# Optimization experiments

Measured on AMD Instinct MI355X. Metric: run time of the kernel, lower is better.

Reference implementation:

```python
import jax, jax.numpy as jnp
import numpy as np

D_MODEL = 2048
N_HEADS = 16
D_HEAD = D_MODEL // N_HEADS
B, S = 4, 2048


def setup_inputs() -> dict:
    key = jax.random.key(0)
    ks = jax.random.split(key, 5)
    scale = 1.0 / np.sqrt(D_MODEL)
    return {
        "x": jax.random.normal(ks[0], (B, S, D_MODEL), dtype=jnp.float32),
        "w_qkv": jax.random.normal(ks[1], (D_MODEL, 3 * D_MODEL), dtype=jnp.float32) * scale,
        "b_qkv": jax.random.normal(ks[2], (3 * D_MODEL,), dtype=jnp.float32) * 0.01,
        "w_out": jax.random.normal(ks[3], (D_MODEL, D_MODEL), dtype=jnp.float32) * scale,
        "b_out": jax.random.normal(ks[4], (D_MODEL,), dtype=jnp.float32) * 0.01,
    }


def reference(x, w_qkv, b_qkv, w_out, b_out):
    b, s, d = x.shape
    qkv = x @ w_qkv + b_qkv                      # [b, s, 3d]
    q, k, v = jnp.split(qkv, 3, axis=-1)
    # [b, h, s, dh]
    q = q.reshape(b, s, N_HEADS, D_HEAD).transpose(0, 2, 1, 3)
    k = k.reshape(b, s, N_HEADS, D_HEAD).transpose(0, 2, 1, 3)
    v = v.reshape(b, s, N_HEADS, D_HEAD).transpose(0, 2, 1, 3)
    # past_kv is None -> s_past == s
    scale = 1.0 / np.sqrt(D_HEAD).astype(np.float32)
    scores = jnp.einsum("bhqd,bhkd->bhqk", q, k) * scale  # [b, h, s, s]
    # causal mask: disallow j > i (diagonal = 1 + s_past - s = 1)
    causal = jnp.tril(jnp.ones((s, s), dtype=bool))
    scores = jnp.where(causal, scores, jnp.float32(-jnp.inf))
    attn = jax.nn.softmax(scores, axis=-1)
    out = jnp.einsum("bhqk,bhkd->bhqd", attn, v)          # [b, h, s, dh]
    out = out.transpose(0, 2, 1, 3).reshape(b, s, d)
    out = out @ w_out + b_out
    return out, k, v
```

## Files before the change

kernel.cpp:

```cpp
#include <hip/hip_runtime.h>
#include <hip/hip_bf16.h>
#include <cstdint>

typedef unsigned short u16;
typedef unsigned int u32;
typedef __attribute__((ext_vector_type(4))) float f32x4;
typedef __attribute__((ext_vector_type(8))) __bf16 bf16x8;

#define DEVFN static __device__ __forceinline__

constexpr int Bb = 4, S = 2048, Dm = 2048, H = 16, DH = 128;
constexpr int M  = Bb * S;
constexpr int N3 = 3 * Dm;
constexpr int KK = 2048;
constexpr float ATTN_SCALE = 0.088388347648318447f;
constexpr float LOG2E = 1.4426950408889634f;

DEVFN u16 f2bf(float f) {
  union { float f; u32 u; } v; v.f = f;
  u32 u = v.u;
  return (u16)((u + 0x7fffu + ((u >> 16) & 1u)) >> 16);
}

DEVFN void async16(const void* g, void* l) {
  __builtin_amdgcn_global_load_lds(
      (__attribute__((address_space(1))) unsigned int*)(g),
      (__attribute__((address_space(3))) unsigned int*)(l), 16, 0, 0);
}


__global__ __launch_bounds__(256) void k_cvt_bf16(const float* __restrict__ in,
                                                  u16* __restrict__ out, int n) {
  int i = (blockIdx.x * 256 + threadIdx.x) * 4;
  if (i < n) {
    float4 f = *(const float4*)(in + i);
    ushort4 o;
    o.x = f2bf(f.x); o.y = f2bf(f.y); o.z = f2bf(f.z); o.w = f2bf(f.w);
    *(ushort4*)(out + i) = o;
  }
}

__global__ __launch_bounds__(256) void k_transpose_bf16(const float* __restrict__ in,
                                                        u16* __restrict__ out,
                                                        int R, int C) {
  __shared__ float tile[32][33];
  int c0 = blockIdx.x * 32, r0 = blockIdx.y * 32;
  int tx = threadIdx.x & 31, ty = threadIdx.x >> 5;
#pragma unroll
  for (int i = 0; i < 4; i++)
    tile[ty + 8 * i][tx] = in[(size_t)(r0 + ty + 8 * i) * C + c0 + tx];
  __syncthreads();
#pragma unroll
  for (int i = 0; i < 4; i++)
    out[(size_t)(c0 + ty + 8 * i) * R + r0 + tx] = f2bf(tile[tx][ty + 8 * i]);
}


#define RA(buf, half) ((buf) * 65536 + (half) * 16384)
#define RB(buf, half) ((buf) * 65536 + 32768 + (half) * 16384)

#define BARRIER() __builtin_amdgcn_s_barrier()
#define LGK0() asm volatile("s_waitcnt lgkmcnt(0)" ::: "memory")
#define VM6() asm volatile("s_waitcnt vmcnt(6)" ::: "memory")
#define VM0() asm volatile("s_waitcnt vmcnt(0)" ::: "memory")

template <int BUF>
DEVFN void ldAall(const char* lds, int wm, int lrow, int lkg, bf16x8 af[2][4][2]) {
  const char* base = lds + RA(BUF, 0) + wm * 16384;
  const int sw = (lrow & 7) << 4;
#pragma unroll
  for (int ms = 0; ms < 2; ms++)
#pragma unroll
    for (int mi = 0; mi < 4; mi++) {
      int row = ms * 64 + mi * 16 + lrow;
#pragma unroll
      for (int kk = 0; kk < 2; kk++)
        af[ms][mi][kk] = *(const bf16x8*)(base + row * 128 +
                                          ((kk * 64 + lkg * 16) ^ sw));
    }
}

template <int BUF, int NS>
DEVFN void ldB(const char* lds, int wn, int lrow, int lkg, bf16x8 b[2][2]) {
  const char* base = lds + RB(BUF, 0) + (wn >> 1) * 16384;
  const int sw = (lrow & 7) << 4;
#pragma unroll
  for (int ni = 0; ni < 2; ni++) {
    int row = (wn & 1) * 64 + NS * 32 + ni * 16 + lrow;
#pragma unroll
    for (int kk = 0; kk < 2; kk++)
      b[ni][kk] = *(const bf16x8*)(base + row * 128 +
                                   ((kk * 64 + lkg * 16) ^ sw));
  }
}

template <int MS, int NS>
DEVFN void mmq(f32x4 acc[8][4], bf16x8 af[4][2], bf16x8 b[2][2]) {
  __builtin_amdgcn_s_setprio(1);
#pragma unroll
  for (int kk = 0; kk < 2; kk++)
#pragma unroll
    for (int mi = 0; mi < 4; mi++)
#pragma unroll
      for (int ni = 0; ni < 2; ni++)
        acc[MS * 4 + mi][NS * 2 + ni] = __builtin_amdgcn_mfma_f32_16x16x32_bf16(
            af[mi][kk], b[ni][kk], acc[MS * 4 + mi][NS * 2 + ni], 0, 0, 0);
  __builtin_amdgcn_s_setprio(0);
}

#define STAGE0(ptr, region)                                             \
  {                                                                     \
    const u16* _q = (ptr);                                              \
    async16(_q, ldsc + (region) + dstoff);                              \
    async16(_q + (size_t)64 * KK, ldsc + (region) + 8192 + dstoff);     \
  }
#define STAGE(p, region) { STAGE0(p, region); p += 64; }

template <int MODE>
__global__ __launch_bounds__(512, 2) void k_gemm(
    const u16* __restrict__ A, const u16* __restrict__ BT,
    const float* __restrict__ bias, float* __restrict__ Cf,
    u16* __restrict__ q_bf, u16* __restrict__ k_bf, u16* __restrict__ v_bfT,
    int N) {
  __shared__ __align__(16) char lds[131072];
  char* ldsc = lds;
  const int tid = threadIdx.x;
  const int wid = tid >> 6, lane = tid & 63;
  const int wm = wid >> 2, wn = wid & 3;
  const int lrow = lane & 15, lkg = lane >> 4;

  const int bid = blockIdx.x;
  const int xcd = bid & 7;
  const int i = bid >> 3;
  const int r = i & 15;
  const int j = i >> 4;
  const int tm0 = (xcd * 4 + (r >> 2)) << 8;
  const int tn0 = (j * 4 + (r & 3)) << 8;

  const int NT = KK >> 6;

  const int srow = tid >> 3;
  const int scol = (((tid & 7) * 16) ^ ((srow & 7) << 4)) >> 1;
  const int dstoff = (tid & ~63) * 16;
  const u16* bA0 = A + (size_t)(tm0 + srow) * KK + scol;
  const u16* bA1 = A + (size_t)(tm0 + 128 + srow) * KK + scol;
  const u16* bB0 = BT + (size_t)(tn0 + srow) * KK + scol;
  const u16* bB1 = BT + (size_t)(tn0 + 128 + srow) * KK + scol;

  f32x4 acc[8][4] = {};

  STAGE0(bA0, RA(0, 0));
  STAGE0(bA1, RA(0, 1));
  STAGE0(bB0, RB(0, 0));
  STAGE0(bB1, RB(0, 1));
  STAGE0(bA0 + 64, RA(1, 0));
  STAGE0(bA1 + 64, RA(1, 1));
  STAGE0(bB0 + 64, RB(1, 0));
  VM6();
  BARRIER();

  const u16* pB1 = bB1 + 64;
  const u16* pA0 = bA0 + 128;
  const u16* pA1 = bA1 + 128;
  const u16* pB0 = bB0 + 128;

  for (int it = 0; it < NT / 2; it++) {
    bf16x8 af[2][4][2], b0[2][2], b1[2][2];

    ldAall<0>(ldsc, wm, lrow, lkg, af);
    ldB<0, 0>(ldsc, wn, lrow, lkg, b0);
    STAGE(pB1, RB(1, 1));
    BARRIER(); LGK0();
    mmq<0, 0>(acc, af[0], b0);
    BARRIER();

    ldB<0, 1>(ldsc, wn, lrow, lkg, b1);
    STAGE(pA0, RA(0, 0));
    BARRIER(); LGK0();
    mmq<0, 1>(acc, af[0], b1);
    BARRIER();

    STAGE(pA1, RA(0, 1));
    BARRIER();
    mmq<1, 0>(acc, af[1], b0);
    BARRIER();

    STAGE(pB0, RB(0, 0));
    VM6();
    BARRIER();
    mmq<1, 1>(acc, af[1], b1);
    BARRIER();

    ldAall<1>(ldsc, wm, lrow, lkg, af);
    ldB<1, 0>(ldsc, wn, lrow, lkg, b0);
    STAGE(pB1, RB(0, 1));
    BARRIER(); LGK0();
    mmq<0, 0>(acc, af[0], b0);
    BARRIER();

    ldB<1, 1>(ldsc, wn, lrow, lkg, b1);
    STAGE(pA0, RA(1, 0));
    BARRIER(); LGK0();
    mmq<0, 1>(acc, af[0], b1);
    BARRIER();

    STAGE(pA1, RA(1, 1));
    BARRIER();
    mmq<1, 0>(acc, af[1], b0);
    BARRIER();

    STAGE(pB0, RB(1, 0));
    VM6();
    BARRIER();
    mmq<1, 1>(acc, af[1], b1);
    BARRIER();
  }
  VM0();

  if (MODE == 0) {
#pragma unroll
    for (int mig = 0; mig < 8; mig++) {
      int row = tm0 + wm * 128 + (mig >> 2) * 64 + (mig & 3) * 16 + lkg * 4;
#pragma unroll
      for (int nig = 0; nig < 4; nig++) {
        int col = tn0 + wn * 64 + (nig >> 1) * 32 + (nig & 1) * 16 + lrow;
        float bv = bias[col];
#pragma unroll
        for (int r2 = 0; r2 < 4; r2++)
          Cf[(size_t)(row + r2) * N + col] = acc[mig][nig][r2] + bv;
      }
    }
  } else {
#pragma unroll
    for (int mig = 0; mig < 8; mig++) {
      int row = tm0 + wm * 128 + (mig >> 2) * 64 + (mig & 3) * 16 + lkg * 4;
#pragma unroll
      for (int nig = 0; nig < 4; nig++) {
        int n = tn0 + wn * 64 + (nig >> 1) * 32 + (nig & 1) * 16 + lrow;
        float bv = bias[n];
        int type = n >> 11;
        int d = n & 2047;
        int h = d >> 7, dh = d & 127;
#pragma unroll
        for (int r2 = 0; r2 < 4; r2++) {
          int rr = row + r2;
          int b = rr >> 11, s = rr & 2047;
          float val = acc[mig][nig][r2] + bv;
          size_t idx = ((size_t)(b * H + h) * S + s) * DH + dh;
          if (type == 0) {
            q_bf[idx] = f2bf(val * ATTN_SCALE);
          } else if (type == 1) {
            Cf[(size_t)M * Dm + idx] = val;
            k_bf[idx] = f2bf(val);
          } else {
            Cf[(size_t)2 * M * Dm + idx] = val;
            v_bfT[((size_t)(b * H + h) * DH + dh) * S + s] = f2bf(val);
          }
        }
      }
    }
  }
}

__global__ __launch_bounds__(256, 2) void k_attn(const u16* __restrict__ q_bf,
                                                 const u16* __restrict__ k_bf,
                                                 const u16* __restrict__ v_bfT,
                                                 u16* __restrict__ attn_bf) {
  __shared__ u16 ldsK[2][64 * 128];
  __shared__ u16 ldsV[2][128 * 64];
  __shared__ u16 ldsP[4][32 * 64];

  const int tid = threadIdx.x;
  const int wid = tid >> 6, lane = tid & 63;
  const int lrow = lane & 15, lkg = lane >> 4;

  const int bid = blockIdx.x;
  const int xcd = bid & 7;
  const int ii = bid >> 3;
  const int bh = xcd * 8 + (ii >> 4);
  const int qi = 15 - (ii & 15);
  const int b = bh >> 4, h = bh & 15;
  const int wq0 = qi * 128 + wid * 32;
  const int swz = (lrow & 7) << 4;

  const u16* qp = q_bf + (size_t)bh * S * DH;
  const u16* kp = k_bf + (size_t)bh * S * DH;
  const u16* vp = v_bfT + (size_t)bh * DH * S;

  bf16x8 qf[2][4];
#pragma unroll
  for (int qt = 0; qt < 2; qt++)
#pragma unroll
    for (int kk = 0; kk < 4; kk++)
      qf[qt][kk] = *(const bf16x8*)(qp + (size_t)(wq0 + qt * 16 + lrow) * DH +
                                    kk * 32 + lkg * 8);

  float mr[2][4], lr[2][4];
#pragma unroll
  for (int qt = 0; qt < 2; qt++)
#pragma unroll
    for (int r = 0; r < 4; r++) { mr[qt][r] = -1e30f; lr[qt][r] = 0.f; }
  f32x4 oacc[2][8] = {};

  const int nkb = qi * 2 + 2;

  auto stage = [&](int kb, int buf) {
#pragma unroll
    for (int i = 0; i < 4; i++) {
      int L = i * 4096 + wid * 1024 + lane * 16;
      int krow = L >> 8, kch = (L >> 4) & 15;
      async16(kp + (size_t)(kb * 64 + krow) * DH + ((kch ^ (krow & 7)) * 8),
              (char*)ldsK[buf] + L);
      int vd = L >> 7, vch = (L >> 4) & 7;
      async16(vp + (size_t)vd * S + kb * 64 + ((vch ^ (vd & 7)) * 8),
              (char*)ldsV[buf] + L);
    }
  };

  stage(0, 0);
  asm volatile("s_waitcnt vmcnt(0)" ::: "memory");
  __builtin_amdgcn_s_barrier();

  int cur = 0;
  for (int kb = 0; kb < nkb; kb++) {
    if (kb + 1 < nkb) stage(kb + 1, cur ^ 1);

    if (kb * 64 <= wq0 + 31) {
      const u16* Kc = ldsK[cur];
      const u16* Vc = ldsV[cur];
      f32x4 sacc[2][4] = {};
      __builtin_amdgcn_s_setprio(1);
#pragma unroll
      for (int kt = 0; kt < 4; kt++)
#pragma unroll
        for (int kk = 0; kk < 4; kk++) {
          bf16x8 kf = *(const bf16x8*)((const char*)Kc +
                        (kt * 16 + lrow) * 256 + ((kk * 64 + lkg * 16) ^ swz));
          sacc[0][kt] = __builtin_amdgcn_mfma_f32_16x16x32_bf16(qf[0][kk], kf,
                                                                sacc[0][kt], 0, 0, 0);
          sacc[1][kt] = __builtin_amdgcn_mfma_f32_16x16x32_bf16(qf[1][kk], kf,
                                                                sacc[1][kt], 0, 0, 0);
        }
      __builtin_amdgcn_s_setprio(0);

      if (kb * 64 + 63 > wq0) {
#pragma unroll
        for (int qt = 0; qt < 2; qt++)
#pragma unroll
          for (int kt = 0; kt < 4; kt++) {
            int k = kb * 64 + kt * 16 + lrow;
#pragma unroll
            for (int r = 0; r < 4; r++)
              if (k > wq0 + qt * 16 + lkg * 4 + r) sacc[qt][kt][r] = -1e30f;
          }
      }

      float pm[2][4];
#pragma unroll
      for (int qt = 0; qt < 2; qt++)
#pragma unroll
        for (int r = 0; r < 4; r++)
          pm[qt][r] = fmaxf(fmaxf(sacc[qt][0][r], sacc[qt][1][r]),
                            fmaxf(sacc[qt][2][r], sacc[qt][3][r]));
#pragma unroll
      for (int off = 1; off < 16; off <<= 1)
#pragma unroll
        for (int qt = 0; qt < 2; qt++)
#pragma unroll
          for (int r = 0; r < 4; r++)
            pm[qt][r] = fmaxf(pm[qt][r], __shfl_xor(pm[qt][r], off, 64));

      float dmax = pm[0][0] - mr[0][0];
#pragma unroll
      for (int qt = 0; qt < 2; qt++)
#pragma unroll
        for (int r = 0; r < 4; r++)
          dmax = fmaxf(dmax, pm[qt][r] - mr[qt][r]);
      if (!__all(dmax <= 8.0f)) {
        float sc[2][4];
#pragma unroll
        for (int qt = 0; qt < 2; qt++)
#pragma unroll
          for (int r = 0; r < 4; r++) {
            float mn = fmaxf(mr[qt][r], pm[qt][r]);
            sc[qt][r] = exp2f((mr[qt][r] - mn) * LOG2E);
            mr[qt][r] = mn;
            lr[qt][r] *= sc[qt][r];
          }
#pragma unroll
        for (int qt = 0; qt < 2; qt++)
#pragma unroll
          for (int nd = 0; nd < 8; nd++)
#pragma unroll
            for (int r = 0; r < 4; r++) oacc[qt][nd][r] *= sc[qt][r];
      }

      float rs[2][4] = {};
#pragma unroll
      for (int qt = 0; qt < 2; qt++)
#pragma unroll
        for (int kt = 0; kt < 4; kt++)
#pragma unroll
          for (int r = 0; r < 4; r++) {
            float p = exp2f((sacc[qt][kt][r] - mr[qt][r]) * LOG2E);
            rs[qt][r] += p;
            int prow = qt * 16 + lkg * 4 + r;
            *(u16*)((char*)ldsP[wid] + prow * 128 +
                    (((kt * 16 + lrow) * 2) ^ ((prow & 7) << 4))) = f2bf(p);
          }
#pragma unroll
      for (int off = 1; off < 16; off <<= 1)
#pragma unroll
        for (int qt = 0; qt < 2; qt++)
#pragma unroll
          for (int r = 0; r < 4; r++)
            rs[qt][r] += __shfl_xor(rs[qt][r], off, 64);
#pragma unroll
      for (int qt = 0; qt < 2; qt++)
#pragma unroll
        for (int r = 0; r < 4; r++)
          lr[qt][r] += rs[qt][r];

      asm volatile("s_waitcnt lgkmcnt(0)" ::: "memory");
      bf16x8 pf[2][2];
#pragma unroll
      for (int qt = 0; qt < 2; qt++)
#pragma unroll
        for (int kk = 0; kk < 2; kk++)
          pf[qt][kk] = *(const bf16x8*)((const char*)ldsP[wid] +
                         (qt * 16 + lrow) * 128 + ((kk * 64 + lkg * 16) ^ swz));
      __builtin_amdgcn_s_setprio(1);
#pragma unroll
      for (int nd = 0; nd < 8; nd++) {
        bf16x8 vf0 = *(const bf16x8*)((const char*)Vc +
                       (nd * 16 + lrow) * 128 + ((lkg * 16) ^ swz));
        bf16x8 vf1 = *(const bf16x8*)((const char*)Vc +
                       (nd * 16 + lrow) * 128 + ((64 + lkg * 16) ^ swz));
#pragma unroll
        for (int qt = 0; qt < 2; qt++) {
          oacc[qt][nd] = __builtin_amdgcn_mfma_f32_16x16x32_bf16(pf[qt][0], vf0,
                                                                 oacc[qt][nd], 0, 0, 0);
          oacc[qt][nd] = __builtin_amdgcn_mfma_f32_16x16x32_bf16(pf[qt][1], vf1,
                                                                 oacc[qt][nd], 0, 0, 0);
        }
      }
      __builtin_amdgcn_s_setprio(0);
    }

    asm volatile("s_waitcnt vmcnt(0)" ::: "memory");
    __builtin_amdgcn_s_barrier();
    cur ^= 1;
  }

#pragma unroll
  for (int qt = 0; qt < 2; qt++) {
    float inv[4];
#pragma unroll
    for (int r = 0; r < 4; r++) inv[r] = 1.0f / lr[qt][r];
#pragma unroll
    for (int nd = 0; nd < 8; nd++)
#pragma unroll
      for (int r = 0; r < 4; r++) {
        int q = wq0 + qt * 16 + lkg * 4 + r;
        size_t idx = ((size_t)(b * S + q) * H + h) * DH + nd * 16 + lrow;
        attn_bf[idx] = f2bf(oacc[qt][nd][r] * inv[r]);
      }
  }
}


extern "C" void kernel_launch(void* const* d_in, const int* in_sizes, int n_in,
                              void* d_out, int out_size, void* d_ws, size_t ws_size,
                              hipStream_t stream) {
  const float* x     = (const float*)d_in[0];
  const float* w_qkv = (const float*)d_in[1];
  const float* b_qkv = (const float*)d_in[2];
  const float* w_out = (const float*)d_in[3];
  const float* b_out = (const float*)d_in[4];
  float* out = (float*)d_out;

  char* ws = (char*)d_ws;
  u16* x_bf    = (u16*)ws; ws += (size_t)M * Dm * 2;
  u16* wqkvT   = (u16*)ws; ws += (size_t)N3 * Dm * 2;
  u16* woutT   = (u16*)ws; ws += (size_t)Dm * Dm * 2;
  u16* q_bf    = (u16*)ws; ws += (size_t)M * Dm * 2;
  u16* k_bf    = (u16*)ws; ws += (size_t)M * Dm * 2;
  u16* v_bfT   = (u16*)ws; ws += (size_t)M * Dm * 2;
  u16* attn_bf = (u16*)ws; ws += (size_t)M * Dm * 2;

  k_cvt_bf16<<<(M * Dm) / 1024, 256, 0, stream>>>(x, x_bf, M * Dm);
  k_transpose_bf16<<<dim3(N3 / 32, Dm / 32), 256, 0, stream>>>(w_qkv, wqkvT, Dm, N3);
  k_transpose_bf16<<<dim3(Dm / 32, Dm / 32), 256, 0, stream>>>(w_out, woutT, Dm, Dm);

  k_gemm<1><<<(N3 / 256) * (M / 256), 512, 0, stream>>>(
      x_bf, wqkvT, b_qkv, out, q_bf, k_bf, v_bfT, N3);

  k_attn<<<S / 128 * Bb * H, 256, 0, stream>>>(q_bf, k_bf, v_bfT, attn_bf);

  k_gemm<0><<<(Dm / 256) * (M / 256), 512, 0, stream>>>(
      attn_bf, woutT, b_out, out, nullptr, nullptr, nullptr, Dm);
}
```

Before: 559.9 us.

## Restructure GEMM main loop into register double-buffered ping-pong pipeline

Rewrites the bf16 GEMM K-loop so LDS fragment reads for the next quadrant are issued into a second register set (afX/afY, bX/bY) while MFMAs run on the current one. It uses partial lgkmcnt/vmcnt waits with scheduling barriers, staggers global-to-LDS staging across the four sub-steps, and drops the extra barrier around each MFMA block. The goal is to hide LDS and global latency behind matrix-core work and cut barrier stalls. In exchange it raises register pressure, and the fixed wait counts and the clamped prefetch indices near the loop end must exactly match the order of outstanding operations.

```diff
diff --git a/kernel.cpp b/kernel.cpp
--- a/kernel.cpp
+++ b/kernel.cpp
@@ -60,24 +60,23 @@
 #define RB(buf, half) ((buf) * 65536 + 32768 + (half) * 16384)
 
 #define BARRIER() __builtin_amdgcn_s_barrier()
-#define LGK0() asm volatile("s_waitcnt lgkmcnt(0)" ::: "memory")
-#define VM6() asm volatile("s_waitcnt vmcnt(6)" ::: "memory")
-#define VM0() asm volatile("s_waitcnt vmcnt(0)" ::: "memory")
-
-template <int BUF>
-DEVFN void ldAall(const char* lds, int wm, int lrow, int lkg, bf16x8 af[2][4][2]) {
+#define LGKM12() { asm volatile("s_waitcnt lgkmcnt(12)" ::: "memory"); __builtin_amdgcn_sched_barrier(0); }
+#define LGKM0()  { asm volatile("s_waitcnt lgkmcnt(0)" ::: "memory"); __builtin_amdgcn_sched_barrier(0); }
+#define VMC4()   { asm volatile("s_waitcnt vmcnt(4)" ::: "memory"); __builtin_amdgcn_sched_barrier(0); }
+#define VMC8()   { asm volatile("s_waitcnt vmcnt(8)" ::: "memory"); __builtin_amdgcn_sched_barrier(0); }
+#define VMC0()   { asm volatile("s_waitcnt vmcnt(0)" ::: "memory"); __builtin_amdgcn_sched_barrier(0); }
+
+template <int BUF, int QUAD>
+DEVFN void ldAq(const char* lds, int wm, int lrow, int lkg, bf16x8 af[4][2]) {
   const char* base = lds + RA(BUF, 0) + wm * 16384;
   const int sw = (lrow & 7) << 4;
 #pragma unroll
-  for (int ms = 0; ms < 2; ms++)
-#pragma unroll
-    for (int mi = 0; mi < 4; mi++) {
-      int row = ms * 64 + mi * 16 + lrow;
-#pragma unroll
-      for (int kk = 0; kk < 2; kk++)
-        af[ms][mi][kk] = *(const bf16x8*)(base + row * 128 +
-                                          ((kk * 64 + lkg * 16) ^ sw));
-    }
+  for (int mi = 0; mi < 4; mi++) {
+    int row = QUAD * 64 + mi * 16 + lrow;
+#pragma unroll
+    for (int kk = 0; kk < 2; kk++)
+      af[mi][kk] = *(const bf16x8*)(base + row * 128 + ((kk * 64 + lkg * 16) ^ sw));
+  }
 }
 
 template <int BUF, int NS>
@@ -89,8 +88,7 @@
     int row = (wn & 1) * 64 + NS * 32 + ni * 16 + lrow;
 #pragma unroll
     for (int kk = 0; kk < 2; kk++)
-      b[ni][kk] = *(const bf16x8*)(base + row * 128 +
-                                   ((kk * 64 + lkg * 16) ^ sw));
+      b[ni][kk] = *(const bf16x8*)(base + row * 128 + ((kk * 64 + lkg * 16) ^ sw));
   }
 }
 
@@ -108,13 +106,10 @@
   __builtin_amdgcn_s_setprio(0);
 }
 
-#define STAGE0(ptr, region)                                             \
-  {                                                                     \
-    const u16* _q = (ptr);                                              \
-    async16(_q, ldsc + (region) + dstoff);                              \
-    async16(_q + (size_t)64 * KK, ldsc + (region) + 8192 + dstoff);     \
-  }
-#define STAGE(p, region) { STAGE0(p, region); p += 64; }
+DEVFN void stage2(const u16* src, char* ldsc, int region, int dstoff) {
+  async16(src, ldsc + region + dstoff);
+  async16(src + (size_t)64 * KK, ldsc + region + 8192 + dstoff);
+}
 
 template <int MODE>
 __global__ __launch_bounds__(512, 2) void k_gemm(
@@ -148,74 +143,74 @@
   const u16* bB1 = BT + (size_t)(tn0 + 128 + srow) * KK + scol;
 
   f32x4 acc[8][4] = {};
-
-  STAGE0(bA0, RA(0, 0));
-  STAGE0(bA1, RA(0, 1));
-  STAGE0(bB0, RB(0, 0));
-  STAGE0(bB1, RB(0, 1));
-  STAGE0(bA0 + 64, RA(1, 0));
-  STAGE0(bA1 + 64, RA(1, 1));
-  STAGE0(bB0 + 64, RB(1, 0));
-  VM6();
+  bf16x8 afX[4][2], afY[4][2], bX[2][2], bY[2][2];
+
+  stage2(bA0, ldsc, RA(0, 0), dstoff);
+  stage2(bA1, ldsc, RA(0, 1), dstoff);
+  stage2(bB0, ldsc, RB(0, 0), dstoff);
+  stage2(bB1, ldsc, RB(0, 1), dstoff);
+  stage2(bA0 + 64, ldsc, RA(1, 0), dstoff);
+  stage2(bA1 + 64, ldsc, RA(1, 1), dstoff);
+  stage2(bB0 + 64, ldsc, RB(1, 0), dstoff);
+  stage2(bB1 + 64, ldsc, RB(1, 1), dstoff);
+  VMC8();
   BARRIER();
-
-  const u16* pB1 = bB1 + 64;
-  const u16* pA0 = bA0 + 128;
-  const u16* pA1 = bA1 + 128;
-  const u16* pB0 = bB0 + 128;
+  ldAq<0, 0>(ldsc, wm, lrow, lkg, afX);
+  ldB<0, 0>(ldsc, wn, lrow, lkg, bX);
 
   for (int it = 0; it < NT / 2; it++) {
-    bf16x8 af[2][4][2], b0[2][2], b1[2][2];
-
-    ldAall<0>(ldsc, wm, lrow, lkg, af);
-    ldB<0, 0>(ldsc, wn, lrow, lkg, b0);
-    STAGE(pB1, RB(1, 1));
-    BARRIER(); LGK0();
-    mmq<0, 0>(acc, af[0], b0);
-    BARRIER();
-
-    ldB<0, 1>(ldsc, wn, lrow, lkg, b1);
-    STAGE(pA0, RA(0, 0));
-    BARRIER(); LGK0();
-    mmq<0, 1>(acc, af[0], b1);
-    BARRIER();
-
-    STAGE(pA1, RA(0, 1));
-    BARRIER();
-    mmq<1, 0>(acc, af[1], b0);
-    BARRIER();
-
-    STAGE(pB0, RB(0, 0));
-    VM6();
-    BARRIER();
-    mmq<1, 1>(acc, af[1], b1);
-    BARRIER();
-
-    ldAall<1>(ldsc, wm, lrow, lkg, af);
-    ldB<1, 0>(ldsc, wn, lrow, lkg, b0);
-    STAGE(pB1, RB(0, 1));
-    BARRIER(); LGK0();
-    mmq<0, 0>(acc, af[0], b0);
-    BARRIER();
-
-    ldB<1, 1>(ldsc, wn, lrow, lkg, b1);
-    STAGE(pA0, RA(1, 0));
-    BARRIER(); LGK0();
-    mmq<0, 1>(acc, af[0], b1);
-    BARRIER();
-
-    STAGE(pA1, RA(1, 1));
-    BARRIER();
-    mmq<1, 0>(acc, af[1], b0);
-    BARRIER();
-
-    STAGE(pB0, RB(1, 0));
-    VM6();
-    BARRIER();
-    mmq<1, 1>(acc, af[1], b1);
-    BARRIER();
-  }
-  VM0();
+    const int u = it * 2;
+    const int t2 = (u + 2 < NT) ? u + 2 : NT - 2;
+    const int t3 = (u + 3 < NT) ? u + 3 : NT - 1;
+
+    ldAq<0, 1>(ldsc, wm, lrow, lkg, afY);
+    ldB<0, 1>(ldsc, wn, lrow, lkg, bY);
+    LGKM12();
+    mmq<0, 0>(acc, afX, bX);
+    LGKM0();
+    BARRIER();
+
+    stage2(bA0 + t2 * 64, ldsc, RA(0, 0), dstoff);
+    stage2(bA1 + t2 * 64, ldsc, RA(0, 1), dstoff);
+    mmq<0, 1>(acc, afX, bY);
+    VMC4();
+    BARRIER();
+
+    ldAq<1, 0>(ldsc, wm, lrow, lkg, afX);
+    stage2(bB0 + t2 * 64, ldsc, RB(0, 0), dstoff);
+    mmq<1, 1>(acc, afY, bY);
+    BARRIER();
+
+    ldB<1, 0>(ldsc, wn, lrow, lkg, bY);
+    stage2(bB1 + t2 * 64, ldsc, RB(0, 1), dstoff);
+    mmq<1, 0>(acc, afY, bX);
+    BARRIER();
+
+    ldAq<1, 1>(ldsc, wm, lrow, lkg, afY);
+    ldB<1, 1>(ldsc, wn, lrow, lkg, bX);
+    LGKM12();
+    mmq<0, 0>(acc, afX, bY);
+    LGKM0();
+    BARRIER();
+
+    stage2(bA0 + t3 * 64, ldsc, RA(1, 0), dstoff);
+    stage2(bA1 + t3 * 64, ldsc, RA(1, 1), dstoff);
+    mmq<0, 1>(acc, afX, bX);
+    VMC4();
+    BARRIER();
+
+    ldAq<0, 0>(ldsc, wm, lrow, lkg, afX);
+    stage2(bB0 + t3 * 64, ldsc, RB(1, 0), dstoff);
+    mmq<1, 1>(acc, afY, bX);
+    BARRIER();
+
+    ldB<0, 0>(ldsc, wn, lrow, lkg, bX);
+    stage2(bB1 + t3 * 64, ldsc, RB(1, 1), dstoff);
+    mmq<1, 0>(acc, afY, bY);
+    BARRIER();
+  }
+  VMC0();
+  LGKM0();
 
   if (MODE == 0) {
 #pragma unroll
```

New measurement: 565.7 us. Within noise of the previous version (+1.0%).
